# Optimization experiments

Hardware: AMD Instinct MI355X
Metric: run time of the kernel (lower is better)

## Reference

```python
import jax, jax.numpy as jnp
import numpy as np

B, N, E, K, DI, DO = 16, 1024, 16, 3, 32, 32


def setup_inputs() -> dict:
    key = jax.random.key(0)
    k1, k2, k3, k4, k5 = jax.random.split(key, 5)
    return {
        "x": jax.random.normal(k1, (B, N, DI), dtype=jnp.float32),
        "all_emb": jax.random.normal(k2, (B, N, E), dtype=jnp.float32),
        "stock_emb": jax.random.normal(k3, (B, N, E), dtype=jnp.float32),
        "weights_pool": jax.random.normal(k4, (E, K, DI, DO), dtype=jnp.float32) * 0.1,
        "bias_pool": jax.random.normal(k5, (E, DO), dtype=jnp.float32) * 0.1,
    }


def reference(x, all_emb, stock_emb, weights_pool, bias_pool):
    # dynamic adjacency: relu(E E^T) then row softmax -> [B, N, N]
    A = jax.nn.relu(jnp.einsum('bne,bme->bnm', all_emb, all_emb))
    S = jax.nn.softmax(A, axis=-1)
    b, n, _ = S.shape
    k_orders = weights_pool.shape[1]
    eye = jnp.broadcast_to(jnp.eye(n, dtype=S.dtype), S.shape)
    # Chebyshev recursion T_0 = I, T_1 = S, T_k = 2 S T_{k-1} - T_{k-2}
    supports = [eye, S]
    for _ in range(2, k_orders):
        supports.append(2.0 * jnp.matmul(S, supports[-1]) - supports[-2])
    cheby = jnp.stack(supports, axis=1)  # [B, K, N, N]
    # graph propagation per Chebyshev order: [B, K, N, dim_in]
    x_g = jnp.einsum('bkij,bjd->bkid', cheby, x)
    # node-specific weights from stock_emb, fused with conv (avoids [B,N,K,I,O]):
    # original: weights = einsum('bni,ikop->bnkop'); out = einsum('bkni,bnkio->bnko').sum(k)
    out = jnp.einsum('bkni,bne,ekio->bno', x_g, stock_emb, weights_pool)
    bias = jnp.einsum('bne,eo->bno', stock_emb, bias_pool)
    return out + bias
```

## Files before the change

kernel.cpp:

```cpp
#include <hip/hip_runtime.h>
#include <stdint.h>

typedef __bf16 bf16x8 __attribute__((ext_vector_type(8)));
typedef __bf16 bf16x4 __attribute__((ext_vector_type(4)));
typedef float  f32x16 __attribute__((ext_vector_type(16)));

constexpr int kB = 16;
constexpr int kN = 1024;

struct bfhl { __bf16 h, l; };
__device__ __forceinline__ bfhl hilo(float v) {
    bfhl r;
    r.h = (__bf16)v;
    r.l = (__bf16)(v - (float)r.h);
    return r;
}

__device__ __forceinline__ int moff(int f, int h, int j) {
    return 16 * f + ((j < 4) ? (4 * h + j) : (4 * h + j + 4));
}


__global__ __launch_bounds__(256) void prep(
    const float* __restrict__ emb, const float* __restrict__ x,
    const float* __restrict__ Wp,
    __bf16* __restrict__ esf, __bf16* __restrict__ vtf1,
    __bf16* __restrict__ xgf, __bf16* __restrict__ wq)
{
    __shared__ float ls[64 * 36];
    const int tid = threadIdx.x;
    const int bid = blockIdx.x;

    if (bid < 256) {
        const int b = bid >> 4, rg = (bid & 15) << 6;
        const int r = tid >> 2, seg = tid & 3;
        float4 v = *(const float4*)(emb + ((size_t)(b * kN + rg + r) * 16 + seg * 4));
        float f[4] = {v.x, v.y, v.z, v.w};
        bf16x4 hi, lo;
        #pragma unroll
        for (int i = 0; i < 4; ++i) { bfhl t = hilo(f[i]); hi[i] = t.h; lo[i] = t.l; }
        const int kt = ((bid & 15) << 1) + (r >> 5);
        const int lane = ((seg >> 1) << 5) + (r & 31);
        const int j0 = (seg & 1) << 2;
        __bf16* base = esf + ((size_t)(b * 32 + kt) * 2) * 512 + lane * 8 + j0;
        *(bf16x4*)base         = hi;
        *(bf16x4*)(base + 512) = lo;
    } else if (bid < 512) {
        const int bb = bid - 256;
        const int b = bb >> 4, n0 = (bb & 15) << 6;
        const float* sB = x + ((size_t)b * kN + n0) * 32;
        #pragma unroll
        for (int it = 0; it < 2; ++it) {
            int f = it * 256 + tid;
            int row = f >> 3, q8 = f & 7;
            float4 v = *(const float4*)(sB + (size_t)row * 32 + q8 * 4);
            *(float4*)(&ls[row * 36 + q8 * 4]) = v;
        }
        __syncthreads();
        {
            const int mt = tid >> 7, fr = (tid >> 6) & 1, l = tid & 63;
            const int d = l & 31, h = l >> 5;
            bf16x8 ov;
            #pragma unroll
            for (int j = 0; j < 8; ++j)
                ov[j] = (__bf16)ls[(mt * 32 + moff(fr, h, j)) * 36 + d];
            *(bf16x8*)(vtf1 + ((size_t)(b * 32 + (n0 >> 5) + mt) * 2 + fr) * 512 + l * 8) = ov;
        }
        #pragma unroll
        for (int mt = 0; mt < 2; ++mt) {
            const int ks = tid >> 7, pl = (tid >> 6) & 1, l = tid & 63;
            const int node = l & 31, h = l >> 5;
            const float* rp = &ls[(mt * 32 + node) * 36 + ks * 16 + 8 * h];
            float4 u0 = *(const float4*)rp;
            float4 u1 = *(const float4*)(rp + 4);
            float u[8] = {u0.x, u0.y, u0.z, u0.w, u1.x, u1.y, u1.z, u1.w};
            bf16x8 ov;
            #pragma unroll
            for (int j = 0; j < 8; ++j) {
                bfhl t = hilo(u[j]);
                ov[j] = pl ? t.l : t.h;
            }
            const int ntile = b * 32 + (n0 >> 5) + mt;
            *(bf16x8*)(xgf + ((size_t)(ntile * 4 + ks) * 2 + pl) * 512 + l * 8) = ov;
        }
    } else {
        int idx = (bid - 512) * 256 + tid;
        if (idx < 6144) {
            int e = idx / 384, rem = idx - e * 384;
            int ks = rem / 64, r2 = rem - ks * 64;
            int o = r2 >> 1, h = r2 & 1;
            int ki0 = ks * 16 + h * 8;
            bf16x8 hi;
            #pragma unroll
            for (int j = 0; j < 8; ++j)
                hi[j] = (__bf16)Wp[(size_t)e * 3072 + (size_t)(ki0 + j) * 32 + o];
            *(bf16x8*)(wq + (size_t)(e * 6 + ks) * 512 + o * 16 + h * 8) = hi;
        }
    }
}

template<int STAGE>
__global__ __launch_bounds__(256, 2) void apply_mfma(
    const __bf16* __restrict__ esf,
    const __bf16* __restrict__ vtin,
    const float*  __restrict__ x,
    __bf16* __restrict__ vtout,
    __bf16* __restrict__ xgf,
    const __bf16* __restrict__ wq,
    const float*  __restrict__ stock,
    const float*  __restrict__ bias,
    float* __restrict__ out)
{
    __shared__ alignas(16) char smem[24576];
    float*  ps  = (float*)smem;
    float*  Ls  = (float*)(smem + 16896);
    float*  yb  = (float*)(smem + 17408);
    __bf16* xg2 = (__bf16*)(smem + 17408);
    float*  s_s = (float*)(smem + 22016);

    const int tid = threadIdx.x;
    const int w = tid >> 6, l = tid & 63;
    const int q = l & 31, h = l >> 5;
    const int b = blockIdx.x >> 5, q0 = (blockIdx.x & 31) << 5;
    const int ntile = blockIdx.x;

    const __bf16* esfB = esf + (size_t)b * 32768;
    const __bf16* vtfB = vtin + (size_t)b * 32768;

    if (STAGE == 2) {
        int r = tid >> 3, e2 = (tid & 7) * 2;
        *(float2*)(s_s + r * 16 + e2) =
            *(const float2*)(stock + (size_t)(b * kN + q0 + r) * 16 + e2);
    }

    bf16x8 bhi = *(const bf16x8*)(esfB + ((size_t)(q0 >> 5) * 2) * 512 + l * 8);
    bf16x8 blo = *(const bf16x8*)(esfB + ((size_t)(q0 >> 5) * 2 + 1) * 512 + l * 8);

    f32x16 acc = {};
    float Lp = 0.f;

    #pragma unroll 2
    for (int it = 0; it < 8; ++it) {
        const int kt = it * 4 + w;
        bf16x8 ahi = *(const bf16x8*)(esfB + ((size_t)kt * 2) * 512 + l * 8);
        bf16x8 alo = *(const bf16x8*)(esfB + ((size_t)kt * 2 + 1) * 512 + l * 8);
        bf16x8 A0  = *(const bf16x8*)(vtfB + ((size_t)kt * 2) * 512 + l * 8);
        bf16x8 A1  = *(const bf16x8*)(vtfB + ((size_t)kt * 2 + 1) * 512 + l * 8);

        f32x16 S = {};
        S = __builtin_amdgcn_mfma_f32_32x32x16_bf16(ahi, bhi, S, 0, 0, 0);
        S = __builtin_amdgcn_mfma_f32_32x32x16_bf16(ahi, blo, S, 0, 0, 0);
        S = __builtin_amdgcn_mfma_f32_32x32x16_bf16(alo, bhi, S, 0, 0, 0);

        float p[16];
        #pragma unroll
        for (int r = 0; r < 16; ++r) {
            p[r] = __expf(fmaxf(S[r], 0.f));
            Lp += p[r];
        }
        bf16x8 P0, P1;
        #pragma unroll
        for (int j = 0; j < 8; ++j) { P0[j] = (__bf16)p[j]; P1[j] = (__bf16)p[8 + j]; }

        acc = __builtin_amdgcn_mfma_f32_32x32x16_bf16(A0, P0, acc, 0, 0, 0);
        acc = __builtin_amdgcn_mfma_f32_32x32x16_bf16(A1, P1, acc, 0, 0, 0);
    }

    Lp += __shfl_xor(Lp, 32);
    #pragma unroll
    for (int r = 0; r < 16; ++r) {
        int d = (r & 3) + 8 * (r >> 2) + 4 * h;
        ps[w * 1056 + d * 33 + q] = acc[r];
    }
    if (l < 32) Ls[w * 32 + l] = Lp;
    __syncthreads();

    const int qq = tid >> 3, dg = tid & 7;
    const float iL = 1.f / (Ls[qq] + Ls[32 + qq] + Ls[64 + qq] + Ls[96 + qq]);
    float yv[4];
    #pragma unroll
    for (int i = 0; i < 4; ++i) {
        int d = dg * 4 + i;
        yv[i] = (ps[d * 33 + qq] + ps[1056 + d * 33 + qq] +
                 ps[2112 + d * 33 + qq] + ps[3168 + d * 33 + qq]) * iL;
    }

    if (STAGE == 1) {
        #pragma unroll
        for (int i = 0; i < 4; ++i) yb[qq * 36 + dg * 4 + i] = yv[i];
        __syncthreads();
        if (tid < 128) {
            const int fr = tid >> 6, l2 = tid & 63;
            const int d = l2 & 31, h2 = l2 >> 5;
            bf16x8 ov;
            #pragma unroll
            for (int j = 0; j < 8; ++j)
                ov[j] = (__bf16)yb[moff(fr, h2, j) * 36 + d];
            *(bf16x8*)(vtout + ((size_t)(b * 32 + (q0 >> 5)) * 2 + fr) * 512 + l2 * 8) = ov;
        }
        {
            const int ks2 = tid >> 7, pl = (tid >> 6) & 1, l2 = tid & 63;
            const int node = l2 & 31, h2 = l2 >> 5;
            const float* rp = &yb[node * 36 + ks2 * 16 + 8 * h2];
            float4 u0 = *(const float4*)rp;
            float4 u1 = *(const float4*)(rp + 4);
            float u[8] = {u0.x, u0.y, u0.z, u0.w, u1.x, u1.y, u1.z, u1.w};
            bf16x8 ov;
            #pragma unroll
            for (int j = 0; j < 8; ++j) {
                bfhl t = hilo(u[j]);
                ov[j] = pl ? t.l : t.h;
            }
            *(bf16x8*)(xgf + ((size_t)(ntile * 4 + 2 + ks2) * 2 + pl) * 512 + l2 * 8) = ov;
        }
    } else {
        {
            float4 xv = *(const float4*)(x + (size_t)(b * kN + q0 + qq) * 32 + dg * 4);
            float g[4] = {2.f * yv[0] - xv.x, 2.f * yv[1] - xv.y,
                          2.f * yv[2] - xv.z, 2.f * yv[3] - xv.w};
            bf16x4 hi, lo;
            #pragma unroll
            for (int i = 0; i < 4; ++i) { bfhl t = hilo(g[i]); hi[i] = t.h; lo[i] = t.l; }
            *(bf16x4*)(xg2 + qq * 36 + dg * 4)        = hi;
            *(bf16x4*)(xg2 + 1152 + qq * 36 + dg * 4) = lo;
        }
        __syncthreads();

        f32x16 acc2[4] = {};
        const int e0 = w * 4;
        const int o = q;

        #pragma unroll
        for (int ks = 0; ks < 6; ++ks) {
            bf16x8 Ah, Al;
            if (ks < 4) {
                Ah = *(const bf16x8*)(xgf + ((size_t)(ntile * 4 + ks) * 2) * 512 + l * 8);
                Al = *(const bf16x8*)(xgf + ((size_t)(ntile * 4 + ks) * 2 + 1) * 512 + l * 8);
            } else {
                const int base = o * 36 + (ks - 4) * 16 + 8 * h;
                bf16x4 a0 = *(const bf16x4*)(xg2 + base);
                bf16x4 a1 = *(const bf16x4*)(xg2 + base + 4);
                bf16x4 b0 = *(const bf16x4*)(xg2 + 1152 + base);
                bf16x4 b1 = *(const bf16x4*)(xg2 + 1152 + base + 4);
                #pragma unroll
                for (int j = 0; j < 4; ++j) {
                    Ah[j] = a0[j]; Ah[4 + j] = a1[j];
                    Al[j] = b0[j]; Al[4 + j] = b1[j];
                }
            }
            #pragma unroll
            for (int ei = 0; ei < 4; ++ei) {
                bf16x8 Bh = *(const bf16x8*)(wq + (size_t)((e0 + ei) * 6 + ks) * 512 + o * 16 + h * 8);
                acc2[ei] = __builtin_amdgcn_mfma_f32_32x32x16_bf16(Ah, Bh, acc2[ei], 0, 0, 0);
                acc2[ei] = __builtin_amdgcn_mfma_f32_32x32x16_bf16(Al, Bh, acc2[ei], 0, 0, 0);
            }
        }

        float pr[16];
        #pragma unroll
        for (int r = 0; r < 16; ++r) pr[r] = 0.f;
        #pragma unroll
        for (int ei = 0; ei < 4; ++ei) {
            const int eg = e0 + ei;
            const float bv = bias[eg * 32 + o];
            #pragma unroll
            for (int r = 0; r < 16; ++r) {
                int node = (r & 3) + 8 * (r >> 2) + 4 * h;
                pr[r] += s_s[node * 16 + eg] * (acc2[ei][r] + bv);
            }
        }
        #pragma unroll
        for (int r = 0; r < 16; ++r) {
            int node = (r & 3) + 8 * (r >> 2) + 4 * h;
            ps[w * 1056 + node * 33 + o] = pr[r];
        }
        __syncthreads();
        {
            const int node = tid >> 3, og = (tid & 7) * 4;
            float4 s;
            #pragma unroll
            for (int i = 0; i < 4; ++i) {
                int c = node * 33 + og + i;
                ((float*)&s)[i] = ps[c] + ps[1056 + c] + ps[2112 + c] + ps[3168 + c];
            }
            *(float4*)(out + (size_t)(b * kN + q0 + node) * 32 + og) = s;
        }
    }
}

extern "C" void kernel_launch(void* const* d_in, const int* in_sizes, int n_in,
                              void* d_out, int out_size, void* d_ws, size_t ws_size,
                              hipStream_t stream) {
    const float* x     = (const float*)d_in[0];
    const float* aemb  = (const float*)d_in[1];
    const float* stock = (const float*)d_in[2];
    const float* Wp    = (const float*)d_in[3];
    const float* bias  = (const float*)d_in[4];
    float* out = (float*)d_out;

    __bf16* wsb  = (__bf16*)d_ws;
    __bf16* esf  = wsb;
    __bf16* vtf1 = wsb + 524288;
    __bf16* vtf2 = wsb + 1048576;
    __bf16* xgf  = wsb + 1572864;
    __bf16* wq   = wsb + 3670016;

    prep<<<dim3(536), dim3(256), 0, stream>>>(aemb, x, Wp, esf, vtf1, xgf, wq);
    apply_mfma<1><<<dim3(512), dim3(256), 0, stream>>>(
        esf, vtf1, x, vtf2, xgf, wq, stock, bias, out);
    apply_mfma<2><<<dim3(512), dim3(256), 0, stream>>>(
        esf, vtf2, x, nullptr, xgf, wq, stock, bias, out);
}
```

Measured before the change: 29.10 us.

## Process two query tiles per block, fold log2e into embeddings, swizzle blocks

Each apply block now has 512 threads and handles two 32-node query tiles, so every key tile's embedding and value fragments it loads feed both tiles. The query embeddings are pre-scaled by log2e in a second buffer, which lets the exponent use exp2f instead of __expf. Block indices are swizzled across batches. Stage 2 builds the x order-0 fragments itself from raw x rather than from a precomputed xgf buffer. In exchange, shared memory per block rises to 56 KB, the grid halves to 256 blocks, and the two tiles are reduced one after the other behind extra barriers.

```diff
diff --git a/kernel.cpp b/kernel.cpp
--- a/kernel.cpp
+++ b/kernel.cpp
@@ -7,6 +7,7 @@
 
 constexpr int kB = 16;
 constexpr int kN = 1024;
+constexpr float kLog2e = 1.44269504088896340736f;
 
 struct bfhl { __bf16 h, l; };
 __device__ __forceinline__ bfhl hilo(float v) {
@@ -24,8 +25,8 @@
 __global__ __launch_bounds__(256) void prep(
     const float* __restrict__ emb, const float* __restrict__ x,
     const float* __restrict__ Wp,
-    __bf16* __restrict__ esf, __bf16* __restrict__ vtf1,
-    __bf16* __restrict__ xgf, __bf16* __restrict__ wq)
+    __bf16* __restrict__ esf, __bf16* __restrict__ esq,
+    __bf16* __restrict__ vtf1, __bf16* __restrict__ wq)
 {
     __shared__ float ls[64 * 36];
     const int tid = threadIdx.x;
@@ -36,15 +37,20 @@
         const int r = tid >> 2, seg = tid & 3;
         float4 v = *(const float4*)(emb + ((size_t)(b * kN + rg + r) * 16 + seg * 4));
         float f[4] = {v.x, v.y, v.z, v.w};
-        bf16x4 hi, lo;
-        #pragma unroll
-        for (int i = 0; i < 4; ++i) { bfhl t = hilo(f[i]); hi[i] = t.h; lo[i] = t.l; }
+        bf16x4 hi, lo, qhi, qlo;
+        #pragma unroll
+        for (int i = 0; i < 4; ++i) {
+            bfhl t = hilo(f[i]);           hi[i] = t.h;  lo[i] = t.l;
+            bfhl s = hilo(f[i] * kLog2e);  qhi[i] = s.h; qlo[i] = s.l;
+        }
         const int kt = ((bid & 15) << 1) + (r >> 5);
         const int lane = ((seg >> 1) << 5) + (r & 31);
         const int j0 = (seg & 1) << 2;
-        __bf16* base = esf + ((size_t)(b * 32 + kt) * 2) * 512 + lane * 8 + j0;
-        *(bf16x4*)base         = hi;
-        *(bf16x4*)(base + 512) = lo;
+        const size_t off = ((size_t)(b * 32 + kt) * 2) * 512 + lane * 8 + j0;
+        *(bf16x4*)(esf + off)       = hi;
+        *(bf16x4*)(esf + off + 512) = lo;
+        *(bf16x4*)(esq + off)       = qhi;
+        *(bf16x4*)(esq + off + 512) = qlo;
     } else if (bid < 512) {
         const int bb = bid - 256;
         const int b = bb >> 4, n0 = (bb & 15) << 6;
@@ -66,65 +72,50 @@
                 ov[j] = (__bf16)ls[(mt * 32 + moff(fr, h, j)) * 36 + d];
             *(bf16x8*)(vtf1 + ((size_t)(b * 32 + (n0 >> 5) + mt) * 2 + fr) * 512 + l * 8) = ov;
         }
-        #pragma unroll
-        for (int mt = 0; mt < 2; ++mt) {
-            const int ks = tid >> 7, pl = (tid >> 6) & 1, l = tid & 63;
-            const int node = l & 31, h = l >> 5;
-            const float* rp = &ls[(mt * 32 + node) * 36 + ks * 16 + 8 * h];
-            float4 u0 = *(const float4*)rp;
-            float4 u1 = *(const float4*)(rp + 4);
-            float u[8] = {u0.x, u0.y, u0.z, u0.w, u1.x, u1.y, u1.z, u1.w};
-            bf16x8 ov;
-            #pragma unroll
-            for (int j = 0; j < 8; ++j) {
-                bfhl t = hilo(u[j]);
-                ov[j] = pl ? t.l : t.h;
-            }
-            const int ntile = b * 32 + (n0 >> 5) + mt;
-            *(bf16x8*)(xgf + ((size_t)(ntile * 4 + ks) * 2 + pl) * 512 + l * 8) = ov;
-        }
     } else {
         int idx = (bid - 512) * 256 + tid;
         if (idx < 6144) {
             int e = idx / 384, rem = idx - e * 384;
             int ks = rem / 64, r2 = rem - ks * 64;
-            int o = r2 >> 1, h = r2 & 1;
-            int ki0 = ks * 16 + h * 8;
+            int o = r2 >> 1, hh = r2 & 1;
+            int ki0 = ks * 16 + hh * 8;
             bf16x8 hi;
             #pragma unroll
             for (int j = 0; j < 8; ++j)
                 hi[j] = (__bf16)Wp[(size_t)e * 3072 + (size_t)(ki0 + j) * 32 + o];
-            *(bf16x8*)(wq + (size_t)(e * 6 + ks) * 512 + o * 16 + h * 8) = hi;
+            *(bf16x8*)(wq + (size_t)(e * 6 + ks) * 512 + o * 16 + hh * 8) = hi;
         }
     }
 }
 
 template<int STAGE>
-__global__ __launch_bounds__(256, 2) void apply_mfma(
-    const __bf16* __restrict__ esf,
+__global__ __launch_bounds__(512, 2) void apply_mfma(
+    const __bf16* __restrict__ esf, const __bf16* __restrict__ esq,
     const __bf16* __restrict__ vtin,
     const float*  __restrict__ x,
-    __bf16* __restrict__ vtout,
-    __bf16* __restrict__ xgf,
+    __bf16* __restrict__ vtout, __bf16* __restrict__ y1f,
     const __bf16* __restrict__ wq,
-    const float*  __restrict__ stock,
-    const float*  __restrict__ bias,
+    const float*  __restrict__ stock, const float* __restrict__ bias,
     float* __restrict__ out)
 {
-    __shared__ alignas(16) char smem[24576];
+    __shared__ alignas(16) char smem[57344];
     float*  ps  = (float*)smem;
-    float*  Ls  = (float*)(smem + 16896);
-    float*  yb  = (float*)(smem + 17408);
-    __bf16* xg2 = (__bf16*)(smem + 17408);
-    float*  s_s = (float*)(smem + 22016);
+    float*  Ls  = (float*)(smem + 33792);
+    float*  yb0 = (float*)(smem + 34816);
+    float*  yb1 = (float*)(smem + 39424);
+    __bf16* xg2 = (__bf16*)(smem + 44032);
+    float*  s_s = (float*)(smem + 53248);
 
     const int tid = threadIdx.x;
     const int w = tid >> 6, l = tid & 63;
     const int q = l & 31, h = l >> 5;
-    const int b = blockIdx.x >> 5, q0 = (blockIdx.x & 31) << 5;
-    const int ntile = blockIdx.x;
+    const int sw = ((blockIdx.x & 7) << 5) + (blockIdx.x >> 3);
+    const int b = sw >> 4, tg = sw & 15;
+    const int q0 = tg << 6;
+    const int nt0 = tg << 1;
 
     const __bf16* esfB = esf + (size_t)b * 32768;
+    const __bf16* esqB = esq + (size_t)b * 32768;
     const __bf16* vtfB = vtin + (size_t)b * 32768;
 
     if (STAGE == 2) {
@@ -133,115 +124,166 @@
             *(const float2*)(stock + (size_t)(b * kN + q0 + r) * 16 + e2);
     }
 
-    bf16x8 bhi = *(const bf16x8*)(esfB + ((size_t)(q0 >> 5) * 2) * 512 + l * 8);
-    bf16x8 blo = *(const bf16x8*)(esfB + ((size_t)(q0 >> 5) * 2 + 1) * 512 + l * 8);
-
-    f32x16 acc = {};
-    float Lp = 0.f;
-
-    #pragma unroll 2
-    for (int it = 0; it < 8; ++it) {
-        const int kt = it * 4 + w;
+    bf16x8 bhi0 = *(const bf16x8*)(esqB + ((size_t)nt0 * 2) * 512 + l * 8);
+    bf16x8 blo0 = *(const bf16x8*)(esqB + ((size_t)nt0 * 2 + 1) * 512 + l * 8);
+    bf16x8 bhi1 = *(const bf16x8*)(esqB + ((size_t)(nt0 + 1) * 2) * 512 + l * 8);
+    bf16x8 blo1 = *(const bf16x8*)(esqB + ((size_t)(nt0 + 1) * 2 + 1) * 512 + l * 8);
+
+    f32x16 acc0 = {}, acc1 = {};
+    float Lp0 = 0.f, Lp1 = 0.f;
+
+    #pragma unroll
+    for (int it = 0; it < 4; ++it) {
+        const int kt = it * 8 + w;
         bf16x8 ahi = *(const bf16x8*)(esfB + ((size_t)kt * 2) * 512 + l * 8);
         bf16x8 alo = *(const bf16x8*)(esfB + ((size_t)kt * 2 + 1) * 512 + l * 8);
         bf16x8 A0  = *(const bf16x8*)(vtfB + ((size_t)kt * 2) * 512 + l * 8);
         bf16x8 A1  = *(const bf16x8*)(vtfB + ((size_t)kt * 2 + 1) * 512 + l * 8);
 
-        f32x16 S = {};
-        S = __builtin_amdgcn_mfma_f32_32x32x16_bf16(ahi, bhi, S, 0, 0, 0);
-        S = __builtin_amdgcn_mfma_f32_32x32x16_bf16(ahi, blo, S, 0, 0, 0);
-        S = __builtin_amdgcn_mfma_f32_32x32x16_bf16(alo, bhi, S, 0, 0, 0);
-
-        float p[16];
+        f32x16 S0 = {}, S1 = {};
+        S0 = __builtin_amdgcn_mfma_f32_32x32x16_bf16(ahi, bhi0, S0, 0, 0, 0);
+        S0 = __builtin_amdgcn_mfma_f32_32x32x16_bf16(ahi, blo0, S0, 0, 0, 0);
+        S0 = __builtin_amdgcn_mfma_f32_32x32x16_bf16(alo, bhi0, S0, 0, 0, 0);
+        S1 = __builtin_amdgcn_mfma_f32_32x32x16_bf16(ahi, bhi1, S1, 0, 0, 0);
+        S1 = __builtin_amdgcn_mfma_f32_32x32x16_bf16(ahi, blo1, S1, 0, 0, 0);
+        S1 = __builtin_amdgcn_mfma_f32_32x32x16_bf16(alo, bhi1, S1, 0, 0, 0);
+
+        float p0[16], p1[16];
         #pragma unroll
         for (int r = 0; r < 16; ++r) {
-            p[r] = __expf(fmaxf(S[r], 0.f));
-            Lp += p[r];
-        }
-        bf16x8 P0, P1;
-        #pragma unroll
-        for (int j = 0; j < 8; ++j) { P0[j] = (__bf16)p[j]; P1[j] = (__bf16)p[8 + j]; }
-
-        acc = __builtin_amdgcn_mfma_f32_32x32x16_bf16(A0, P0, acc, 0, 0, 0);
-        acc = __builtin_amdgcn_mfma_f32_32x32x16_bf16(A1, P1, acc, 0, 0, 0);
-    }
-
-    Lp += __shfl_xor(Lp, 32);
+            p0[r] = exp2f(fmaxf(S0[r], 0.f));  Lp0 += p0[r];
+            p1[r] = exp2f(fmaxf(S1[r], 0.f));  Lp1 += p1[r];
+        }
+        bf16x8 P00, P01, P10, P11;
+        #pragma unroll
+        for (int j = 0; j < 8; ++j) {
+            P00[j] = (__bf16)p0[j]; P01[j] = (__bf16)p0[8 + j];
+            P10[j] = (__bf16)p1[j]; P11[j] = (__bf16)p1[8 + j];
+        }
+        acc0 = __builtin_amdgcn_mfma_f32_32x32x16_bf16(A0, P00, acc0, 0, 0, 0);
+        acc0 = __builtin_amdgcn_mfma_f32_32x32x16_bf16(A1, P01, acc0, 0, 0, 0);
+        acc1 = __builtin_amdgcn_mfma_f32_32x32x16_bf16(A0, P10, acc1, 0, 0, 0);
+        acc1 = __builtin_amdgcn_mfma_f32_32x32x16_bf16(A1, P11, acc1, 0, 0, 0);
+    }
+
+    Lp0 += __shfl_xor(Lp0, 32);
     #pragma unroll
     for (int r = 0; r < 16; ++r) {
         int d = (r & 3) + 8 * (r >> 2) + 4 * h;
-        ps[w * 1056 + d * 33 + q] = acc[r];
-    }
-    if (l < 32) Ls[w * 32 + l] = Lp;
+        ps[w * 1056 + d * 33 + q] = acc0[r];
+    }
+    if (l < 32) Ls[w * 32 + l] = Lp0;
     __syncthreads();
-
-    const int qq = tid >> 3, dg = tid & 7;
-    const float iL = 1.f / (Ls[qq] + Ls[32 + qq] + Ls[64 + qq] + Ls[96 + qq]);
-    float yv[4];
+    {
+        const int qq = tid >> 4, dgi = tid & 15;
+        float Lsum = 0.f;
+        #pragma unroll
+        for (int k = 0; k < 8; ++k) Lsum += Ls[k * 32 + qq];
+        const float iL = 1.f / Lsum;
+        #pragma unroll
+        for (int i = 0; i < 2; ++i) {
+            int d = dgi * 2 + i;
+            float s = 0.f;
+            #pragma unroll
+            for (int k = 0; k < 8; ++k) s += ps[k * 1056 + d * 33 + qq];
+            yb0[qq * 36 + d] = s * iL;
+        }
+    }
+    __syncthreads();
+    Lp1 += __shfl_xor(Lp1, 32);
     #pragma unroll
-    for (int i = 0; i < 4; ++i) {
-        int d = dg * 4 + i;
-        yv[i] = (ps[d * 33 + qq] + ps[1056 + d * 33 + qq] +
-                 ps[2112 + d * 33 + qq] + ps[3168 + d * 33 + qq]) * iL;
-    }
+    for (int r = 0; r < 16; ++r) {
+        int d = (r & 3) + 8 * (r >> 2) + 4 * h;
+        ps[w * 1056 + d * 33 + q] = acc1[r];
+    }
+    if (l < 32) Ls[w * 32 + l] = Lp1;
+    __syncthreads();
+    {
+        const int qq = tid >> 4, dgi = tid & 15;
+        float Lsum = 0.f;
+        #pragma unroll
+        for (int k = 0; k < 8; ++k) Lsum += Ls[k * 32 + qq];
+        const float iL = 1.f / Lsum;
+        #pragma unroll
+        for (int i = 0; i < 2; ++i) {
+            int d = dgi * 2 + i;
+            float s = 0.f;
+            #pragma unroll
+            for (int k = 0; k < 8; ++k) s += ps[k * 1056 + d * 33 + qq];
+            yb1[qq * 36 + d] = s * iL;
+        }
+    }
+    __syncthreads();
 
     if (STAGE == 1) {
-        #pragma unroll
-        for (int i = 0; i < 4; ++i) yb[qq * 36 + dg * 4 + i] = yv[i];
-        __syncthreads();
-        if (tid < 128) {
-            const int fr = tid >> 6, l2 = tid & 63;
-            const int d = l2 & 31, h2 = l2 >> 5;
+        if (tid < 256) {
+            int t = tid >> 7, fr = (tid >> 6) & 1, l2 = tid & 63;
+            int d = l2 & 31, h2 = l2 >> 5;
+            const float* yb = t ? yb1 : yb0;
             bf16x8 ov;
             #pragma unroll
             for (int j = 0; j < 8; ++j)
                 ov[j] = (__bf16)yb[moff(fr, h2, j) * 36 + d];
-            *(bf16x8*)(vtout + ((size_t)(b * 32 + (q0 >> 5)) * 2 + fr) * 512 + l2 * 8) = ov;
+            *(bf16x8*)(vtout + ((size_t)(b * 32 + nt0 + t) * 2 + fr) * 512 + l2 * 8) = ov;
         }
         {
-            const int ks2 = tid >> 7, pl = (tid >> 6) & 1, l2 = tid & 63;
-            const int node = l2 & 31, h2 = l2 >> 5;
-            const float* rp = &yb[node * 36 + ks2 * 16 + 8 * h2];
-            float4 u0 = *(const float4*)rp;
-            float4 u1 = *(const float4*)(rp + 4);
-            float u[8] = {u0.x, u0.y, u0.z, u0.w, u1.x, u1.y, u1.z, u1.w};
+            int t = tid >> 8, rest = tid & 255;
+            int ks2 = rest >> 7, pl = (rest >> 6) & 1, l2 = rest & 63;
+            int node = l2 & 31, h2 = l2 >> 5;
+            const float* yb = t ? yb1 : yb0;
+            const float* rp = yb + node * 36 + ks2 * 16 + 8 * h2;
             bf16x8 ov;
             #pragma unroll
             for (int j = 0; j < 8; ++j) {
-                bfhl t = hilo(u[j]);
-                ov[j] = pl ? t.l : t.h;
-            }
-            *(bf16x8*)(xgf + ((size_t)(ntile * 4 + 2 + ks2) * 2 + pl) * 512 + l2 * 8) = ov;
+                bfhl tt = hilo(rp[j]);
+                ov[j] = pl ? tt.l : tt.h;
+            }
+            *(bf16x8*)(y1f + (((size_t)(b * 32 + nt0 + t) * 2 + ks2) * 2 + pl) * 512 + l2 * 8) = ov;
         }
     } else {
         {
-            float4 xv = *(const float4*)(x + (size_t)(b * kN + q0 + qq) * 32 + dg * 4);
-            float g[4] = {2.f * yv[0] - xv.x, 2.f * yv[1] - xv.y,
-                          2.f * yv[2] - xv.z, 2.f * yv[3] - xv.w};
+            int node = tid >> 3, dg = tid & 7;
+            int t = node >> 5, nl = node & 31;
+            const float* yb = t ? yb1 : yb0;
+            float4 xv = *(const float4*)(x + (size_t)(b * kN + q0 + node) * 32 + dg * 4);
+            float xa[4] = {xv.x, xv.y, xv.z, xv.w};
             bf16x4 hi, lo;
             #pragma unroll
-            for (int i = 0; i < 4; ++i) { bfhl t = hilo(g[i]); hi[i] = t.h; lo[i] = t.l; }
-            *(bf16x4*)(xg2 + qq * 36 + dg * 4)        = hi;
-            *(bf16x4*)(xg2 + 1152 + qq * 36 + dg * 4) = lo;
+            for (int i = 0; i < 4; ++i) {
+                float y2v = yb[nl * 36 + dg * 4 + i];
+                bfhl tt = hilo(2.f * y2v - xa[i]);
+                hi[i] = tt.h; lo[i] = tt.l;
+            }
+            *(bf16x4*)(xg2 + node * 36 + dg * 4)        = hi;
+            *(bf16x4*)(xg2 + 2304 + node * 36 + dg * 4) = lo;
         }
         __syncthreads();
 
         f32x16 acc2[4] = {};
-        const int e0 = w * 4;
+        const int t = w >> 2;
+        const int e0 = (w & 3) * 4;
         const int o = q;
+        const int gnt = b * 32 + nt0 + t;
 
         #pragma unroll
         for (int ks = 0; ks < 6; ++ks) {
             bf16x8 Ah, Al;
-            if (ks < 4) {
-                Ah = *(const bf16x8*)(xgf + ((size_t)(ntile * 4 + ks) * 2) * 512 + l * 8);
-                Al = *(const bf16x8*)(xgf + ((size_t)(ntile * 4 + ks) * 2 + 1) * 512 + l * 8);
+            if (ks < 2) {
+                const float* rp = x + (size_t)(b * kN + q0 + t * 32 + q) * 32 + ks * 16 + 8 * h;
+                float4 u0 = *(const float4*)rp;
+                float4 u1 = *(const float4*)(rp + 4);
+                float u[8] = {u0.x, u0.y, u0.z, u0.w, u1.x, u1.y, u1.z, u1.w};
+                #pragma unroll
+                for (int j = 0; j < 8; ++j) { bfhl tt = hilo(u[j]); Ah[j] = tt.h; Al[j] = tt.l; }
+            } else if (ks < 4) {
+                Ah = *(const bf16x8*)(y1f + (((size_t)gnt * 2 + (ks - 2)) * 2 + 0) * 512 + l * 8);
+                Al = *(const bf16x8*)(y1f + (((size_t)gnt * 2 + (ks - 2)) * 2 + 1) * 512 + l * 8);
             } else {
-                const int base = o * 36 + (ks - 4) * 16 + 8 * h;
+                const int base = (t * 32 + o) * 36 + (ks - 4) * 16 + 8 * h;
                 bf16x4 a0 = *(const bf16x4*)(xg2 + base);
                 bf16x4 a1 = *(const bf16x4*)(xg2 + base + 4);
-                bf16x4 b0 = *(const bf16x4*)(xg2 + 1152 + base);
-                bf16x4 b1 = *(const bf16x4*)(xg2 + 1152 + base + 4);
+                bf16x4 b0 = *(const bf16x4*)(xg2 + 2304 + base);
+                bf16x4 b1 = *(const bf16x4*)(xg2 + 2304 + base + 4);
                 #pragma unroll
                 for (int j = 0; j < 4; ++j) {
                     Ah[j] = a0[j]; Ah[4 + j] = a1[j];
@@ -265,23 +307,25 @@
             const float bv = bias[eg * 32 + o];
             #pragma unroll
             for (int r = 0; r < 16; ++r) {
-                int node = (r & 3) + 8 * (r >> 2) + 4 * h;
-                pr[r] += s_s[node * 16 + eg] * (acc2[ei][r] + bv);
+                int nl = (r & 3) + 8 * (r >> 2) + 4 * h;
+                pr[r] += s_s[(t * 32 + nl) * 16 + eg] * (acc2[ei][r] + bv);
             }
         }
         #pragma unroll
         for (int r = 0; r < 16; ++r) {
-            int node = (r & 3) + 8 * (r >> 2) + 4 * h;
-            ps[w * 1056 + node * 33 + o] = pr[r];
+            int nl = (r & 3) + 8 * (r >> 2) + 4 * h;
+            ps[w * 1056 + nl * 33 + o] = pr[r];
         }
         __syncthreads();
         {
             const int node = tid >> 3, og = (tid & 7) * 4;
+            const int tt = node >> 5;
             float4 s;
             #pragma unroll
             for (int i = 0; i < 4; ++i) {
-                int c = node * 33 + og + i;
-                ((float*)&s)[i] = ps[c] + ps[1056 + c] + ps[2112 + c] + ps[3168 + c];
+                int c = (node & 31) * 33 + og + i;
+                ((float*)&s)[i] = ps[(tt * 4 + 0) * 1056 + c] + ps[(tt * 4 + 1) * 1056 + c] +
+                                  ps[(tt * 4 + 2) * 1056 + c] + ps[(tt * 4 + 3) * 1056 + c];
             }
             *(float4*)(out + (size_t)(b * kN + q0 + node) * 32 + og) = s;
         }
@@ -300,14 +344,15 @@
 
     __bf16* wsb  = (__bf16*)d_ws;
     __bf16* esf  = wsb;
-    __bf16* vtf1 = wsb + 524288;
-    __bf16* vtf2 = wsb + 1048576;
-    __bf16* xgf  = wsb + 1572864;
-    __bf16* wq   = wsb + 3670016;
-
-    prep<<<dim3(536), dim3(256), 0, stream>>>(aemb, x, Wp, esf, vtf1, xgf, wq);
-    apply_mfma<1><<<dim3(512), dim3(256), 0, stream>>>(
-        esf, vtf1, x, vtf2, xgf, wq, stock, bias, out);
-    apply_mfma<2><<<dim3(512), dim3(256), 0, stream>>>(
-        esf, vtf2, x, nullptr, xgf, wq, stock, bias, out);
-}
+    __bf16* esq  = wsb + 524288;
+    __bf16* vtf1 = wsb + 1048576;
+    __bf16* vtf2 = wsb + 1572864;
+    __bf16* y1f  = wsb + 2097152;
+    __bf16* wq   = wsb + 3145728;
+
+    prep<<<dim3(536), dim3(256), 0, stream>>>(aemb, x, Wp, esf, esq, vtf1, wq);
+    apply_mfma<1><<<dim3(256), dim3(512), 0, stream>>>(
+        esf, esq, vtf1, x, vtf2, y1f, wq, stock, bias, out);
+    apply_mfma<2><<<dim3(256), dim3(512), 0, stream>>>(
+        esf, esq, vtf2, x, nullptr, y1f, wq, stock, bias, out);
+}
```

New measurement: 31.26 us. +7.4%, slower.
